# Kernel tuning notes

Measured on AMD Instinct MI355X. Metric: run time of the kernel, lower is better.

## Reference

```python
import jax, jax.numpy as jnp
import numpy as np

OUTPUT_SIZES = [1, 3, 6, 8]  # SPP pyramid -> total KV length 110

def _bounds(n, out):
    # PyTorch AdaptiveMaxPool2d bin boundaries
    return [((i * n) // out, -((-(i + 1) * n) // out)) for i in range(out)]

def adaptive_max_pool2d(x, out):
    # x: [B, C, H, W] -> [B, C, out, out]
    B, C, H, W = x.shape
    rows = jnp.stack([x[:, :, s:e, :].max(axis=2) for s, e in _bounds(H, out)], axis=2)
    return jnp.stack([rows[:, :, :, s:e].max(axis=3) for s, e in _bounds(W, out)], axis=3)

def spp(x):
    # [B, C, H, W] -> [B, C, S] with S = sum(o*o) = 110
    B, C = x.shape[:2]
    return jnp.concatenate(
        [adaptive_max_pool2d(x, o).reshape(B, C, o * o) for o in OUTPUT_SIZES], axis=2)

def conv1x1(x, w):
    # 1x1 conv, no bias: w [O, C], x [B, C, H, W]
    return jnp.einsum('oc,bchw->bohw', w, x)

def setup_inputs() -> dict:
    key = jax.random.key(0)
    ks = jax.random.split(key, 6)
    B, C, H, W = 16, 512, 64, 64
    IC = C // 2
    x = jax.random.normal(ks[0], (B, C, H, W), jnp.float32)
    y = jax.random.normal(ks[1], (B, C, H, W), jnp.float32)
    sc = 1.0 / np.sqrt(C)
    w_phi = jax.random.normal(ks[2], (IC, C), jnp.float32) * sc
    w_theta = jax.random.normal(ks[3], (IC, C), jnp.float32) * sc
    w_g = jax.random.normal(ks[4], (IC, C), jnp.float32) * sc
    w_mask = jax.random.normal(ks[5], (C, IC), jnp.float32) * (1.0 / np.sqrt(IC))
    return {"x": x, "y": y, "w_phi": w_phi, "w_theta": w_theta,
            "w_g": w_g, "w_mask": w_mask}

def reference(x, y, w_phi, w_theta, w_g, w_mask):
    B, C, H, W = x.shape
    IC = w_phi.shape[0]
    N = H * W
    # Query: [B, N, IC]
    x_phi = conv1x1(x, w_phi).reshape(B, IC, N).transpose(0, 2, 1)
    # Keys/values from SPP-pooled y: [B, IC, S] / [B, S, IC]
    y_theta = spp(conv1x1(y, w_theta))
    y_g = spp(conv1x1(y, w_g)).transpose(0, 2, 1)
    # Attention with softmax over the QUERY axis (dim=1), as in the source
    attn = jax.nn.softmax(jnp.einsum('bnc,bcs->bns', x_phi, y_theta), axis=1)
    agg = jnp.einsum('bns,bsc->bnc', attn, y_g)          # [B, N, IC]
    agg = agg.transpose(0, 2, 1).reshape(B, IC, H, W)     # [B, IC, H, W]
    mask = conv1x1(agg, w_mask)                           # [B, C, H, W]
    return mask + x
```

## Files before the change

### kernel.cpp

```cpp
#include <hip/hip_runtime.h>

#define DI __device__ __forceinline__

typedef __attribute__((ext_vector_type(8))) __bf16 bf16x8;
typedef __attribute__((ext_vector_type(4))) float f32x4;

DI unsigned short f2bf(float x) {
  union { float f; unsigned u; } v; v.f = x;
  unsigned r = v.u + 0x7fffu + ((v.u >> 16) & 1u);
  return (unsigned short)(r >> 16);
}
DI float bf2f(unsigned short h) {
  union { unsigned u; float f; } v; v.u = ((unsigned)h) << 16;
  return v.f;
}
DI unsigned pack2(float a, float b) {
  return (unsigned)f2bf(a) | (((unsigned)f2bf(b)) << 16);
}

DI void gl_lds16(const void* g, void* l) {
  __builtin_amdgcn_global_load_lds(
      (const __attribute__((address_space(1))) void*)g,
      (__attribute__((address_space(3))) void*)l, 16, 0, 0);
}

__global__ __launch_bounds__(256) void p0w_transpose(
    const float* __restrict__ src, unsigned short* __restrict__ dst,
    const float* __restrict__ w_theta, const float* __restrict__ w_g,
    unsigned short* __restrict__ wTG)
{
  if (blockIdx.z == 16) {
    if (blockIdx.y < 2) {
      int e = ((blockIdx.y * 64 + blockIdx.x) * 256 + threadIdx.x) * 8;
      const float* s = (e < 131072) ? (w_theta + e) : (w_g + (e - 131072));
      float4 a = *(const float4*)s;
      float4 c = *(const float4*)(s + 4);
      uint4 u;
      u.x = pack2(a.x, a.y); u.y = pack2(a.z, a.w);
      u.z = pack2(c.x, c.y); u.w = pack2(c.z, c.w);
      *(uint4*)(wTG + e) = u;
    }
    return;
  }
  const int n0 = blockIdx.x * 64, c0 = blockIdx.y * 64, b = blockIdx.z;
  const int tid = threadIdx.x;
  __shared__ float T[64 * 65];
  #pragma unroll
  for (int p = 0; p < 4; ++p) {
    int r = p * 16 + (tid >> 4);
    int n4 = (tid & 15) << 2;
    *(float4*)&T[r * 65 + n4] =
        *(const float4*)(src + ((size_t)(b * 512 + c0 + r)) * 4096 + n0 + n4);
  }
  __syncthreads();
  int n = tid >> 2, cc = (tid & 3) * 16;
  unsigned u[8];
  #pragma unroll
  for (int j = 0; j < 16; j += 2)
    u[j >> 1] = pack2(T[(cc + j) * 65 + n], T[(cc + j + 1) * 65 + n]);
  unsigned short* d = dst + ((size_t)(b * 4096 + n0 + n)) * 512 + c0 + cc;
  *(uint4*)(d) = make_uint4(u[0], u[1], u[2], u[3]);
  *(uint4*)(d + 8) = make_uint4(u[4], u[5], u[6], u[7]);
}

__constant__ int c_RS[18] = {0, 0,21,42, 0,10,21,32,42,53, 0,8,16,24,32,40,48,56};
__constant__ int c_RE[18] = {64, 22,43,64, 11,22,32,43,54,64, 8,16,24,32,40,48,56,64};

__global__ __launch_bounds__(256) void k1f_conv_pool(
    const unsigned short* __restrict__ yT, const unsigned short* __restrict__ wTG,
    unsigned short* __restrict__ Rbuf)
{
  const int tid = threadIdx.x;
  const int id = blockIdx.x;
  const int tile = (id & 7) * 16 + (id >> 3);
  const int mb = (tile & 3) * 128;
  const int nbt = tile >> 2;
  const int nb = nbt * 128;
  const int b  = blockIdx.y;
  const int lane = tid & 63, wv = tid >> 6;
  const int wm = (wv & 1) * 64, wn = (wv >> 1) * 64;
  const int l15 = lane & 15, l4 = lane >> 4;

  __shared__ __align__(16) char smem[33280];
  float* P = (float*)smem;

  f32x4 acc[4][4];
  #pragma unroll
  for (int i = 0; i < 4; ++i)
    #pragma unroll
    for (int j = 0; j < 4; ++j) acc[i][j] = f32x4{0.f, 0.f, 0.f, 0.f};

  auto stage = [&](int buf, int kb) {
    unsigned short* As = (unsigned short*)(smem + buf * 16384);
    unsigned short* Bs = As + 4096;
    #pragma unroll
    for (int p = 0; p < 2; ++p) {
      int chunk = (wv * 2 + p) * 64 + lane;
      int row = chunk >> 2, c16 = chunk & 3;
      gl_lds16(wTG + ((size_t)(mb + row)) * 512 + kb + c16 * 8,
               As + (wv * 2 + p) * 512);
      gl_lds16(yT + ((size_t)(b * 4096 + nb + row)) * 512 + kb + c16 * 8,
               Bs + (wv * 2 + p) * 512);
    }
  };

  stage(0, 0);
  __syncthreads();
  int cur = 0;
  for (int t = 0; t < 16; ++t) {
    if (t < 15) stage(cur ^ 1, (t + 1) * 32);
    const unsigned short* As = (const unsigned short*)(smem + cur * 16384);
    const unsigned short* Bs = As + 4096;
    bf16x8 af[4], bfr[4];
    #pragma unroll
    for (int i = 0; i < 4; ++i)
      af[i] = *(const bf16x8*)&As[(wm + i * 16 + l15) * 32 + l4 * 8];
    #pragma unroll
    for (int j = 0; j < 4; ++j)
      bfr[j] = *(const bf16x8*)&Bs[(wn + j * 16 + l15) * 32 + l4 * 8];
    #pragma unroll
    for (int i = 0; i < 4; ++i)
      #pragma unroll
      for (int j = 0; j < 4; ++j)
        acc[i][j] = __builtin_amdgcn_mfma_f32_16x16x32_bf16(af[i], bfr[j], acc[i][j], 0, 0, 0);
    __syncthreads();
    cur ^= 1;
  }

  const int hloc = wv >> 1;
  #pragma unroll
  for (int pass = 0; pass < 2; ++pass) {
    __syncthreads();
    if (hloc == pass) {
      #pragma unroll
      for (int i = 0; i < 4; ++i)
        #pragma unroll
        for (int j = 0; j < 4; ++j)
          #pragma unroll
          for (int r = 0; r < 4; ++r)
            P[(wm + i * 16 + l4 * 4 + r) * 65 + j * 16 + l15] = acc[i][j][r];
    }
    __syncthreads();
    const int o = tid & 127;
    size_t rbase = (((size_t)(b * 64 + nbt * 2 + pass)) * 18) * 512 + mb + o;
    if (tid < 128) {
      float b0 = -3.4e38f, b1 = b0, b2 = b0, b3 = b0;
      #pragma unroll
      for (int w = 0; w < 64; ++w) {
        float v = P[o * 65 + w];
        b0 = fmaxf(b0, v);
        if (w < 22) b1 = fmaxf(b1, v);
        if (w >= 21 && w < 43) b2 = fmaxf(b2, v);
        if (w >= 42) b3 = fmaxf(b3, v);
      }
      Rbuf[rbase]           = f2bf(b0);
      Rbuf[rbase + 512]     = f2bf(b1);
      Rbuf[rbase + 2 * 512] = f2bf(b2);
      Rbuf[rbase + 3 * 512] = f2bf(b3);
    } else {
      float s6[6], s8[8];
      #pragma unroll
      for (int i = 0; i < 6; ++i) s6[i] = -3.4e38f;
      #pragma unroll
      for (int i = 0; i < 8; ++i) s8[i] = -3.4e38f;
      constexpr int R6S[6] = {0, 10, 21, 32, 42, 53};
      constexpr int R6E[6] = {11, 22, 32, 43, 54, 64};
      #pragma unroll
      for (int w = 0; w < 64; ++w) {
        float v = P[o * 65 + w];
        #pragma unroll
        for (int i = 0; i < 6; ++i)
          if (w >= R6S[i] && w < R6E[i]) s6[i] = fmaxf(s6[i], v);
        s8[w >> 3] = fmaxf(s8[w >> 3], v);
      }
      #pragma unroll
      for (int i = 0; i < 6; ++i) Rbuf[rbase + (size_t)(4 + i) * 512] = f2bf(s6[i]);
      #pragma unroll
      for (int i = 0; i < 8; ++i) Rbuf[rbase + (size_t)(10 + i) * 512] = f2bf(s8[i]);
    }
  }
}

__global__ __launch_bounds__(256) void k2_pool_final(
    const unsigned short* __restrict__ Rbuf, float* __restrict__ Pt,
    float* __restrict__ Pg)
{
  const int s = blockIdx.x, b = blockIdx.y, tid = threadIdx.x;
  size_t obase = ((size_t)(b * 128) + s) * 256 + tid;
  if (s >= 110) { Pt[obase] = 0.f; Pg[obase] = 0.f; return; }
  int he, wb;
  if (s == 0)      { he = 0; wb = 0; }
  else if (s < 10) { int i = s - 1;  he = 1 + i / 3;  wb = 1 + i % 3; }
  else if (s < 46) { int i = s - 10; he = 4 + i / 6;  wb = 4 + i % 6; }
  else             { int i = s - 46; he = 10 + i / 8; wb = 10 + i % 8; }
  float m0 = -3.4e38f, m1 = -3.4e38f;
  int e = c_RE[he];
  for (int h = c_RS[he]; h < e; ++h) {
    const unsigned short* r = Rbuf + (((size_t)(b * 64 + h)) * 18 + wb) * 512;
    m0 = fmaxf(m0, bf2f(r[tid]));
    m1 = fmaxf(m1, bf2f(r[tid + 256]));
  }
  Pt[obase] = m0;
  Pg[obase] = m1;
}

__global__ __launch_bounds__(256) void k3_fused(
    const float* __restrict__ Pt, const float* __restrict__ Pg,
    const float* __restrict__ w_phi, const float* __restrict__ w_mask,
    unsigned short* __restrict__ Kth, unsigned short* __restrict__ Ktl,
    unsigned short* __restrict__ Vb)
{
  __shared__ __align__(16) char sm3[51200];
  const int tid = threadIdx.x;
  const int tx = tid & 15, ty = tid >> 4;
  const int b = blockIdx.y;
  if (blockIdx.z == 0) {
    const int ct = blockIdx.x;
    const int c0 = tx * 4, s0 = ty * 8;
    float* Ls = (float*)sm3;
    float* Ws = Ls + 128 * 64;
    float acc[8][4] = {};
    for (int kc = 0; kc < 256; kc += 64) {
      #pragma unroll
      for (int j = 0; j < 8; ++j) {
        int flat = tid + 256 * j;
        int row = flat >> 4, k4 = (flat & 15) << 2;
        *(float4*)&Ls[row * 64 + k4] =
            *(const float4*)(Pt + ((size_t)(b * 128) + row) * 256 + kc + k4);
      }
      #pragma unroll
      for (int j = 0; j < 4; ++j) {
        int flat = tid + 256 * j;
        int row = flat >> 4, c4 = (flat & 15) << 2;
        *(float4*)&Ws[row * 68 + c4] =
            *(const float4*)(w_phi + (size_t)(kc + row) * 512 + ct * 64 + c4);
      }
      __syncthreads();
      for (int k = 0; k < 64; k += 4) {
        float4 wv[4];
        #pragma unroll
        for (int kk = 0; kk < 4; ++kk) wv[kk] = *(const float4*)&Ws[(k + kk) * 68 + c0];
        #pragma unroll
        for (int i = 0; i < 8; ++i) {
          float4 a = *(const float4*)&Ls[(s0 + i) * 64 + k];
          const float* ap = (const float*)&a;
          #pragma unroll
          for (int kk = 0; kk < 4; ++kk) {
            const float* wp = (const float*)&wv[kk];
            acc[i][0] += ap[kk] * wp[0];
            acc[i][1] += ap[kk] * wp[1];
            acc[i][2] += ap[kk] * wp[2];
            acc[i][3] += ap[kk] * wp[3];
          }
        }
      }
      __syncthreads();
    }
    #pragma unroll
    for (int i = 0; i < 8; ++i) {
      unsigned short hi[4]; float lo[4];
      #pragma unroll
      for (int j = 0; j < 4; ++j) { hi[j] = f2bf(acc[i][j]); lo[j] = acc[i][j] - bf2f(hi[j]); }
      size_t base = ((size_t)(b * 128) + s0 + i) * 512 + ct * 64 + c0;
      uint2 uh; uh.x = (unsigned)hi[0] | ((unsigned)hi[1] << 16);
      uh.y = (unsigned)hi[2] | ((unsigned)hi[3] << 16);
      uint2 ul; ul.x = pack2(lo[0], lo[1]); ul.y = pack2(lo[2], lo[3]);
      *(uint2*)&Kth[base] = uh;
      *(uint2*)&Ktl[base] = ul;
    }
  } else {
    const int ot = blockIdx.x;
    const int o0 = ty * 4;
    float* Ws = (float*)sm3;
    float* Ps = Ws + 64 * 64;
    float acc[4][8] = {};
    for (int kc = 0; kc < 256; kc += 64) {
      #pragma unroll
      for (int j = 0; j < 4; ++j) {
        int flat = tid + 256 * j;
        int row = flat >> 4, k4 = (flat & 15) << 2;
        *(float4*)&Ws[row * 64 + k4] =
            *(const float4*)(w_mask + (size_t)(ot * 64 + row) * 256 + kc + k4);
      }
      #pragma unroll
      for (int j = 0; j < 8; ++j) {
        int flat = tid + 256 * j;
        int row = flat >> 4, k4 = (flat & 15) << 2;
        *(float4*)&Ps[row * 68 + k4] =
            *(const float4*)(Pg + ((size_t)(b * 128) + row) * 256 + kc + k4);
      }
      __syncthreads();
      for (int k = 0; k < 64; k += 4) {
        float4 wv[4];
        #pragma unroll
        for (int i = 0; i < 4; ++i) wv[i] = *(const float4*)&Ws[(o0 + i) * 64 + k];
        #pragma unroll
        for (int jj = 0; jj < 8; ++jj) {
          float4 pv = *(const float4*)&Ps[(tx + 16 * jj) * 68 + k];
          const float* pp = (const float*)&pv;
          #pragma unroll
          for (int i = 0; i < 4; ++i) {
            const float* wp = (const float*)&wv[i];
            #pragma unroll
            for (int kk = 0; kk < 4; ++kk) acc[i][jj] += wp[kk] * pp[kk];
          }
        }
      }
      __syncthreads();
    }
    #pragma unroll
    for (int i = 0; i < 4; ++i)
      #pragma unroll
      for (int jj = 0; jj < 8; ++jj)
        Vb[((size_t)(b * 512) + ot * 64 + o0 + i) * 128 + tx + 16 * jj] =
            f2bf(acc[i][jj]);
  }
}

__global__ __launch_bounds__(256) void k4_scores(
    const unsigned short* __restrict__ xT, const unsigned short* __restrict__ Kth,
    const unsigned short* __restrict__ Ktl, float* __restrict__ scores,
    float* __restrict__ pmax_g, float* __restrict__ psum_g)
{
  const int tid = threadIdx.x;
  const int ntile = blockIdx.x;
  const int nb = ntile * 128;
  const int b = blockIdx.y;
  const int lane = tid & 63, wv = tid >> 6;
  const int wm = (wv & 1) * 64, wn = (wv >> 1) * 64;
  const int l15 = lane & 15, l4 = lane >> 4;
  __shared__ __align__(16) char smem4[49152];
  __shared__ float SmP[256], SsP[256];
  f32x4 acc[4][4];
  #pragma unroll
  for (int i = 0; i < 4; ++i)
    #pragma unroll
    for (int j = 0; j < 4; ++j) acc[i][j] = f32x4{0.f, 0.f, 0.f, 0.f};

  auto stage = [&](int buf, int kb) {
    unsigned short* Ah = (unsigned short*)(smem4 + buf * 24576);
    unsigned short* Al = Ah + 4096;
    unsigned short* Bs = Al + 4096;
    #pragma unroll
    for (int p = 0; p < 2; ++p) {
      int chunk = (wv * 2 + p) * 64 + lane;
      int row = chunk >> 2, c16 = chunk & 3;
      size_t g = ((size_t)(b * 128) + row) * 512 + kb + c16 * 8;
      gl_lds16(Kth + g, Ah + (wv * 2 + p) * 512);
      gl_lds16(Ktl + g, Al + (wv * 2 + p) * 512);
      gl_lds16(xT + ((size_t)(b * 4096 + nb + row)) * 512 + kb + c16 * 8,
               Bs + (wv * 2 + p) * 512);
    }
  };

  stage(0, 0);
  __syncthreads();
  int cur = 0;
  for (int t = 0; t < 16; ++t) {
    if (t < 15) stage(cur ^ 1, (t + 1) * 32);
    const unsigned short* Ah = (const unsigned short*)(smem4 + cur * 24576);
    const unsigned short* Al = Ah + 4096;
    const unsigned short* Bs = Al + 4096;
    bf16x8 ah[4], al[4], bfr[4];
    #pragma unroll
    for (int i = 0; i < 4; ++i) {
      ah[i] = *(const bf16x8*)&Ah[(wm + i * 16 + l15) * 32 + l4 * 8];
      al[i] = *(const bf16x8*)&Al[(wm + i * 16 + l15) * 32 + l4 * 8];
    }
    #pragma unroll
    for (int j = 0; j < 4; ++j)
      bfr[j] = *(const bf16x8*)&Bs[(wn + j * 16 + l15) * 32 + l4 * 8];
    #pragma unroll
    for (int i = 0; i < 4; ++i)
      #pragma unroll
      for (int j = 0; j < 4; ++j) {
        acc[i][j] = __builtin_amdgcn_mfma_f32_16x16x32_bf16(ah[i], bfr[j], acc[i][j], 0, 0, 0);
        acc[i][j] = __builtin_amdgcn_mfma_f32_16x16x32_bf16(al[i], bfr[j], acc[i][j], 0, 0, 0);
      }
    __syncthreads();
    cur ^= 1;
  }

  #pragma unroll
  for (int i = 0; i < 4; ++i)
    #pragma unroll
    for (int j = 0; j < 4; ++j)
      #pragma unroll
      for (int r = 0; r < 4; ++r)
        scores[((size_t)(b * 128) + wm + i * 16 + l4 * 4 + r) * 4096 + nb + wn + j * 16 + l15] =
            acc[i][j][r];

  const int nh = wn >> 6;
  float cm[4][4];
  #pragma unroll
  for (int i = 0; i < 4; ++i)
    #pragma unroll
    for (int r = 0; r < 4; ++r) {
      float v = fmaxf(fmaxf(acc[i][0][r], acc[i][1][r]),
                      fmaxf(acc[i][2][r], acc[i][3][r]));
      v = fmaxf(v, __shfl_xor(v, 1));
      v = fmaxf(v, __shfl_xor(v, 2));
      v = fmaxf(v, __shfl_xor(v, 4));
      v = fmaxf(v, __shfl_xor(v, 8));
      if (l15 == 0) SmP[(wm + i * 16 + l4 * 4 + r) * 2 + nh] = v;
    }
  __syncthreads();
  #pragma unroll
  for (int i = 0; i < 4; ++i)
    #pragma unroll
    for (int r = 0; r < 4; ++r) {
      int s = wm + i * 16 + l4 * 4 + r;
      cm[i][r] = fmaxf(SmP[s * 2], SmP[s * 2 + 1]);
    }
  #pragma unroll
  for (int i = 0; i < 4; ++i)
    #pragma unroll
    for (int r = 0; r < 4; ++r) {
      float s0 = __expf(acc[i][0][r] - cm[i][r]) + __expf(acc[i][1][r] - cm[i][r]) +
                 __expf(acc[i][2][r] - cm[i][r]) + __expf(acc[i][3][r] - cm[i][r]);
      s0 += __shfl_xor(s0, 1);
      s0 += __shfl_xor(s0, 2);
      s0 += __shfl_xor(s0, 4);
      s0 += __shfl_xor(s0, 8);
      if (l15 == 0) SsP[(wm + i * 16 + l4 * 4 + r) * 2 + nh] = s0;
    }
  __syncthreads();
  if (tid < 128) {
    size_t pidx = ((size_t)(b * 128) + tid) * 32 + ntile;
    pmax_g[pidx] = fmaxf(SmP[tid * 2], SmP[tid * 2 + 1]);
    psum_g[pidx] = SsP[tid * 2] + SsP[tid * 2 + 1];
  }
}

__global__ __launch_bounds__(256) void k5e_expT(
    const float* __restrict__ scores, const float* __restrict__ pmax_g,
    const float* __restrict__ psum_g, unsigned short* __restrict__ Eb)
{
  const int nt = blockIdx.x, b = blockIdx.y, tid = threadIdx.x;
  __shared__ float L[128 * 68];
  __shared__ float sm[128], sl[128];
  if (tid < 128) {
    float M = 0.f, linv = 0.f;
    if (tid < 110) {
      const float* pm = pmax_g + ((size_t)(b * 128) + tid) * 32;
      const float* ps = psum_g + ((size_t)(b * 128) + tid) * 32;
      M = -3.4e38f;
      #pragma unroll
      for (int t = 0; t < 32; ++t) M = fmaxf(M, pm[t]);
      float S = 0.f;
      #pragma unroll
      for (int t = 0; t < 32; ++t) S += ps[t] * __expf(pm[t] - M);
      linv = 1.f / S;
    }
    sm[tid] = M; sl[tid] = linv;
  }
  #pragma unroll
  for (int j = 0; j < 8; ++j) {
    int flat = tid + 256 * j;
    int s = flat >> 4, n4 = (flat & 15) << 2;
    *(float4*)&L[s * 68 + n4] =
        *(const float4*)(scores + ((size_t)(b * 128) + s) * 4096 + nt * 64 + n4);
  }
  __syncthreads();
  int n = tid >> 2, sq = (tid & 3) * 32;
  unsigned ub[16];
  #pragma unroll
  for (int k = 0; k < 32; k += 2) {
    float e0 = __expf(L[(sq + k) * 68 + n] - sm[sq + k]) * sl[sq + k];
    float e1 = __expf(L[(sq + k + 1) * 68 + n] - sm[sq + k + 1]) * sl[sq + k + 1];
    ub[k >> 1] = pack2(e0, e1);
  }
  uint4* dst = (uint4*)(Eb + ((size_t)(b * 4096) + nt * 64 + n) * 128 + sq);
  #pragma unroll
  for (int j = 0; j < 4; ++j)
    dst[j] = make_uint4(ub[4 * j], ub[4 * j + 1], ub[4 * j + 2], ub[4 * j + 3]);
}

__global__ __launch_bounds__(256) void k6_out(
    const unsigned short* __restrict__ Eb, const unsigned short* __restrict__ Vb,
    const float* __restrict__ x, float* __restrict__ out)
{
  const int tid = threadIdx.x;
  const int nb = blockIdx.x * 128;
  const int mb = blockIdx.y * 128;
  const int b = blockIdx.z;
  const int lane = tid & 63, wv = tid >> 6;
  const int wm = (wv & 1) * 64, wn = (wv >> 1) * 64;
  const int l15 = lane & 15, l4 = lane >> 4;
  __shared__ __align__(16) unsigned short SA[4][4096];
  __shared__ __align__(16) unsigned short SB[4][4096];

  #pragma unroll
  for (int h = 0; h < 4; ++h)
    #pragma unroll
    for (int p = 0; p < 2; ++p) {
      int chunk = (wv * 2 + p) * 64 + lane;
      int row = chunk >> 2, c16 = chunk & 3;
      gl_lds16(Vb + ((size_t)(b * 512) + mb + row) * 128 + h * 32 + c16 * 8,
               &SA[h][(wv * 2 + p) * 512]);
      gl_lds16(Eb + ((size_t)(b * 4096) + nb + row) * 128 + h * 32 + c16 * 8,
               &SB[h][(wv * 2 + p) * 512]);
    }

  float xr[4][4][4];
  #pragma unroll
  for (int i = 0; i < 4; ++i)
    #pragma unroll
    for (int j = 0; j < 4; ++j)
      #pragma unroll
      for (int r = 0; r < 4; ++r)
        xr[i][j][r] = x[((size_t)(b * 512) + mb + wm + i * 16 + l4 * 4 + r) * 4096 +
                        nb + wn + j * 16 + l15];

  f32x4 acc[4][4];
  #pragma unroll
  for (int i = 0; i < 4; ++i)
    #pragma unroll
    for (int j = 0; j < 4; ++j) acc[i][j] = f32x4{0.f, 0.f, 0.f, 0.f};

  __syncthreads();
  #pragma unroll
  for (int h = 0; h < 4; ++h) {
    bf16x8 af[4], bfr[4];
    #pragma unroll
    for (int i = 0; i < 4; ++i)
      af[i] = *(const bf16x8*)&SA[h][(wm + i * 16 + l15) * 32 + l4 * 8];
    #pragma unroll
    for (int j = 0; j < 4; ++j)
      bfr[j] = *(const bf16x8*)&SB[h][(wn + j * 16 + l15) * 32 + l4 * 8];
    #pragma unroll
    for (int i = 0; i < 4; ++i)
      #pragma unroll
      for (int j = 0; j < 4; ++j)
        acc[i][j] = __builtin_amdgcn_mfma_f32_16x16x32_bf16(af[i], bfr[j], acc[i][j], 0, 0, 0);
  }
  #pragma unroll
  for (int i = 0; i < 4; ++i)
    #pragma unroll
    for (int j = 0; j < 4; ++j)
      #pragma unroll
      for (int r = 0; r < 4; ++r) {
        int o = mb + wm + i * 16 + l4 * 4 + r;
        size_t idx = ((size_t)(b * 512) + o) * 4096 + nb + wn + j * 16 + l15;
        out[idx] = acc[i][j][r] + xr[i][j][r];
      }
}

extern "C" void kernel_launch(void* const* d_in, const int* in_sizes, int n_in,
                              void* d_out, int out_size, void* d_ws, size_t ws_size,
                              hipStream_t stream)
{
  (void)in_sizes; (void)n_in; (void)out_size; (void)ws_size;
  const float* x       = (const float*)d_in[0];
  const float* y       = (const float*)d_in[1];
  const float* w_phi   = (const float*)d_in[2];
  const float* w_theta = (const float*)d_in[3];
  const float* w_g     = (const float*)d_in[4];
  const float* w_mask  = (const float*)d_in[5];
  float* out = (float*)d_out;

  char* ws = (char*)d_ws;
  unsigned short* yT = (unsigned short*)ws;
  unsigned short* xT = yT;
  char* B0 = ws + 67108864;
  unsigned short* Rbuf = (unsigned short*)B0;
  float* scores = (float*)B0;
  unsigned short* Eb = (unsigned short*)(B0 + 33554432);
  unsigned short* wTG = (unsigned short*)(B0 + 50331648);
  unsigned short* Vb  = (unsigned short*)(B0 + 50331648);
  float* pmax_g = (float*)(B0 + 52428800);
  float* psum_g = (float*)(B0 + 52690944);
  char* C0 = B0 + 54525952;
  float* Pt = (float*)C0;
  float* Pg = (float*)(C0 + 2097152);
  unsigned short* Kth = (unsigned short*)(C0 + 4194304);
  unsigned short* Ktl = (unsigned short*)(C0 + 6291456);

  p0w_transpose<<<dim3(64, 8, 17), 256, 0, stream>>>(y, yT, w_theta, w_g, wTG);
  k1f_conv_pool<<<dim3(128, 16), 256, 0, stream>>>(yT, wTG, Rbuf);
  k2_pool_final<<<dim3(128, 16), 256, 0, stream>>>(Rbuf, Pt, Pg);
  k3_fused<<<dim3(8, 16, 2), 256, 0, stream>>>(Pt, Pg, w_phi, w_mask, Kth, Ktl, Vb);
  p0w_transpose<<<dim3(64, 8, 16), 256, 0, stream>>>(x, xT, w_theta, w_g, wTG);
  k4_scores<<<dim3(32, 16), 256, 0, stream>>>(xT, Kth, Ktl, scores, pmax_g, psum_g);
  k5e_expT<<<dim3(64, 16), 256, 0, stream>>>(scores, pmax_g, psum_g, Eb);
  k6_out<<<dim3(32, 4, 16), 256, 0, stream>>>(Eb, Vb, x, out);
}
```

Measured before the change: 501.3 us.

## Fuse x transpose/bf16 conversion into scores kernel and store scores transposed

The scores kernel now reads fp32 x directly in its native [C,N] layout, converts it to bf16 in registers and writes it into padded LDS, so the separate x transpose pass and its 64MB-scale bf16 intermediate are removed. Scores are stored in transposed [N,S] order with float4 writes, which lets the exp/normalize kernel become a simple streaming elementwise pass without an LDS transpose. In exchange the x loads are register-staged strided global loads rather than async DMA, which could expose latency in the GEMM loop.

```diff
diff --git a/kernel.cpp b/kernel.cpp
--- a/kernel.cpp
+++ b/kernel.cpp
@@ -318,8 +318,8 @@
 }
 
 __global__ __launch_bounds__(256) void k4_scores(
-    const unsigned short* __restrict__ xT, const unsigned short* __restrict__ Kth,
-    const unsigned short* __restrict__ Ktl, float* __restrict__ scores,
+    const float* __restrict__ x, const unsigned short* __restrict__ Kth,
+    const unsigned short* __restrict__ Ktl, float* __restrict__ scoresT,
     float* __restrict__ pmax_g, float* __restrict__ psum_g)
 {
   const int tid = threadIdx.x;
@@ -329,18 +329,27 @@
   const int lane = tid & 63, wv = tid >> 6;
   const int wm = (wv & 1) * 64, wn = (wv >> 1) * 64;
   const int l15 = lane & 15, l4 = lane >> 4;
-  __shared__ __align__(16) char smem4[49152];
+  __shared__ __align__(16) char smem4[2 * 26624];
   __shared__ float SmP[256], SsP[256];
+
+  const int xn = tid & 127, xh = tid >> 7;
+  const float* xcol = x + ((size_t)(b * 512 + xh * 16)) * 4096 + nb + xn;
+
   f32x4 acc[4][4];
   #pragma unroll
   for (int i = 0; i < 4; ++i)
     #pragma unroll
     for (int j = 0; j < 4; ++j) acc[i][j] = f32x4{0.f, 0.f, 0.f, 0.f};
 
-  auto stage = [&](int buf, int kb) {
-    unsigned short* Ah = (unsigned short*)(smem4 + buf * 24576);
+  float xr[16];
+  auto xload = [&](int kb) {
+    const float* p = xcol + (size_t)kb * 4096;
+    #pragma unroll
+    for (int k = 0; k < 16; ++k) xr[k] = p[(size_t)k * 4096];
+  };
+  auto dmaA = [&](int buf, int kb) {
+    unsigned short* Ah = (unsigned short*)(smem4 + buf * 26624);
     unsigned short* Al = Ah + 4096;
-    unsigned short* Bs = Al + 4096;
     #pragma unroll
     for (int p = 0; p < 2; ++p) {
       int chunk = (wv * 2 + p) * 64 + lane;
@@ -348,19 +357,28 @@
       size_t g = ((size_t)(b * 128) + row) * 512 + kb + c16 * 8;
       gl_lds16(Kth + g, Ah + (wv * 2 + p) * 512);
       gl_lds16(Ktl + g, Al + (wv * 2 + p) * 512);
-      gl_lds16(xT + ((size_t)(b * 4096 + nb + row)) * 512 + kb + c16 * 8,
-               Bs + (wv * 2 + p) * 512);
     }
   };
-
-  stage(0, 0);
+  auto bwrite = [&](int buf) {
+    unsigned short* Bs = (unsigned short*)(smem4 + buf * 26624 + 16384);
+    unsigned u[8];
+    #pragma unroll
+    for (int k = 0; k < 16; k += 2) u[k >> 1] = pack2(xr[k], xr[k + 1]);
+    uint4* d = (uint4*)&Bs[xn * 40 + xh * 16];
+    d[0] = make_uint4(u[0], u[1], u[2], u[3]);
+    d[1] = make_uint4(u[4], u[5], u[6], u[7]);
+  };
+
+  xload(0);
+  dmaA(0, 0);
+  bwrite(0);
   __syncthreads();
   int cur = 0;
   for (int t = 0; t < 16; ++t) {
-    if (t < 15) stage(cur ^ 1, (t + 1) * 32);
-    const unsigned short* Ah = (const unsigned short*)(smem4 + cur * 24576);
+    if (t < 15) { xload((t + 1) * 32); dmaA(cur ^ 1, (t + 1) * 32); }
+    const unsigned short* Ah = (const unsigned short*)(smem4 + cur * 26624);
     const unsigned short* Al = Ah + 4096;
-    const unsigned short* Bs = Al + 4096;
+    const unsigned short* Bs = (const unsigned short*)(smem4 + cur * 26624 + 16384);
     bf16x8 ah[4], al[4], bfr[4];
     #pragma unroll
     for (int i = 0; i < 4; ++i) {
@@ -369,7 +387,7 @@
     }
     #pragma unroll
     for (int j = 0; j < 4; ++j)
-      bfr[j] = *(const bf16x8*)&Bs[(wn + j * 16 + l15) * 32 + l4 * 8];
+      bfr[j] = *(const bf16x8*)&Bs[(wn + j * 16 + l15) * 40 + l4 * 8];
     #pragma unroll
     for (int i = 0; i < 4; ++i)
       #pragma unroll
@@ -377,6 +395,7 @@
         acc[i][j] = __builtin_amdgcn_mfma_f32_16x16x32_bf16(ah[i], bfr[j], acc[i][j], 0, 0, 0);
         acc[i][j] = __builtin_amdgcn_mfma_f32_16x16x32_bf16(al[i], bfr[j], acc[i][j], 0, 0, 0);
       }
+    if (t < 15) bwrite(cur ^ 1);
     __syncthreads();
     cur ^= 1;
   }
@@ -385,10 +404,8 @@
   for (int i = 0; i < 4; ++i)
     #pragma unroll
     for (int j = 0; j < 4; ++j)
-      #pragma unroll
-      for (int r = 0; r < 4; ++r)
-        scores[((size_t)(b * 128) + wm + i * 16 + l4 * 4 + r) * 4096 + nb + wn + j * 16 + l15] =
-            acc[i][j][r];
+      *(float4*)(scoresT + ((size_t)(b * 4096) + nb + wn + j * 16 + l15) * 128 +
+                 wm + i * 16 + l4 * 4) = *(float4*)&acc[i][j];
 
   const int nh = wn >> 6;
   float cm[4][4];
@@ -432,12 +449,11 @@
   }
 }
 
-__global__ __launch_bounds__(256) void k5e_expT(
-    const float* __restrict__ scores, const float* __restrict__ pmax_g,
+__global__ __launch_bounds__(256) void k5e_exp(
+    const float* __restrict__ scoresT, const float* __restrict__ pmax_g,
     const float* __restrict__ psum_g, unsigned short* __restrict__ Eb)
 {
-  const int nt = blockIdx.x, b = blockIdx.y, tid = threadIdx.x;
-  __shared__ float L[128 * 68];
+  const int b = blockIdx.y, tid = threadIdx.x;
   __shared__ float sm[128], sl[128];
   if (tid < 128) {
     float M = 0.f, linv = 0.f;
@@ -454,26 +470,20 @@
     }
     sm[tid] = M; sl[tid] = linv;
   }
+  __syncthreads();
+  const size_t base = (size_t)b * 4096 * 128;
   #pragma unroll
   for (int j = 0; j < 8; ++j) {
-    int flat = tid + 256 * j;
-    int s = flat >> 4, n4 = (flat & 15) << 2;
-    *(float4*)&L[s * 68 + n4] =
-        *(const float4*)(scores + ((size_t)(b * 128) + s) * 4096 + nt * 64 + n4);
-  }
-  __syncthreads();
-  int n = tid >> 2, sq = (tid & 3) * 32;
-  unsigned ub[16];
-  #pragma unroll
-  for (int k = 0; k < 32; k += 2) {
-    float e0 = __expf(L[(sq + k) * 68 + n] - sm[sq + k]) * sl[sq + k];
-    float e1 = __expf(L[(sq + k + 1) * 68 + n] - sm[sq + k + 1]) * sl[sq + k + 1];
-    ub[k >> 1] = pack2(e0, e1);
-  }
-  uint4* dst = (uint4*)(Eb + ((size_t)(b * 4096) + nt * 64 + n) * 128 + sq);
-  #pragma unroll
-  for (int j = 0; j < 4; ++j)
-    dst[j] = make_uint4(ub[4 * j], ub[4 * j + 1], ub[4 * j + 2], ub[4 * j + 3]);
+    int chunk = blockIdx.x * 2048 + j * 256 + tid;
+    int sc = (chunk & 31) * 4;
+    float4 v = *(const float4*)(scoresT + base + (size_t)chunk * 4);
+    float e0 = __expf(v.x - sm[sc])     * sl[sc];
+    float e1 = __expf(v.y - sm[sc + 1]) * sl[sc + 1];
+    float e2 = __expf(v.z - sm[sc + 2]) * sl[sc + 2];
+    float e3 = __expf(v.w - sm[sc + 3]) * sl[sc + 3];
+    uint2 u; u.x = pack2(e0, e1); u.y = pack2(e2, e3);
+    *(uint2*)(Eb + base + (size_t)chunk * 4) = u;
+  }
 }
 
 __global__ __launch_bounds__(256) void k6_out(
@@ -561,10 +571,9 @@
 
   char* ws = (char*)d_ws;
   unsigned short* yT = (unsigned short*)ws;
-  unsigned short* xT = yT;
   char* B0 = ws + 67108864;
   unsigned short* Rbuf = (unsigned short*)B0;
-  float* scores = (float*)B0;
+  float* scoresT = (float*)B0;
   unsigned short* Eb = (unsigned short*)(B0 + 33554432);
   unsigned short* wTG = (unsigned short*)(B0 + 50331648);
   unsigned short* Vb  = (unsigned short*)(B0 + 50331648);
@@ -580,8 +589,7 @@
   k1f_conv_pool<<<dim3(128, 16), 256, 0, stream>>>(yT, wTG, Rbuf);
   k2_pool_final<<<dim3(128, 16), 256, 0, stream>>>(Rbuf, Pt, Pg);
   k3_fused<<<dim3(8, 16, 2), 256, 0, stream>>>(Pt, Pg, w_phi, w_mask, Kth, Ktl, Vb);
-  p0w_transpose<<<dim3(64, 8, 16), 256, 0, stream>>>(x, xT, w_theta, w_g, wTG);
-  k4_scores<<<dim3(32, 16), 256, 0, stream>>>(xT, Kth, Ktl, scores, pmax_g, psum_g);
-  k5e_expT<<<dim3(64, 16), 256, 0, stream>>>(scores, pmax_g, psum_g, Eb);
+  k4_scores<<<dim3(32, 16), 256, 0, stream>>>(x, Kth, Ktl, scoresT, pmax_g, psum_g);
+  k5e_exp<<<dim3(64, 16), 256, 0, stream>>>(scoresT, pmax_g, psum_g, Eb);
   k6_out<<<dim3(32, 4, 16), 256, 0, stream>>>(Eb, Vb, x, out);
 }
```

Result: faster. 490.4 us (-2.2%).
